# Kernel tuning notes

Measured on AMD Instinct MI355X. Metric: run time of the kernel, lower is better.

Reference implementation:

```python
import jax, jax.numpy as jnp
import numpy as np

N2 = 524288   # raw batch (2B)
F = 256       # raw feature dim; concat of halves -> D = 2F
D = 512       # input_dim (gated feature dim)
H_GATE = 64
H_EXP = 128


def _init(key, shape, fan_in):
    return jax.random.normal(key, shape, jnp.float32) / np.sqrt(fan_in)


def setup_inputs() -> dict:
    key = jax.random.key(0)
    ks = jax.random.split(key, 13)
    x = jax.random.normal(ks[0], (N2, F), jnp.float32)
    # gate: Linear(D,64) -> ReLU -> Linear(64,2)
    gw1 = _init(ks[1], (D, H_GATE), D)
    gb1 = jnp.zeros((H_GATE,), jnp.float32)
    gw2 = _init(ks[2], (H_GATE, 2), H_GATE)
    gb2 = jnp.zeros((2,), jnp.float32)
    # expert_a: Linear(D,128) -> ReLU -> Linear(128,2)
    aw1 = _init(ks[3], (D, H_EXP), D)
    ab1 = jnp.zeros((H_EXP,), jnp.float32)
    aw2 = _init(ks[4], (H_EXP, 2), H_EXP)
    ab2 = jnp.zeros((2,), jnp.float32)
    # expert_b: same shapes
    bw1 = _init(ks[5], (D, H_EXP), D)
    bb1 = jnp.zeros((H_EXP,), jnp.float32)
    bw2 = _init(ks[6], (H_EXP, 2), H_EXP)
    bb2 = jnp.zeros((2,), jnp.float32)
    return dict(x=x, gw1=gw1, gb1=gb1, gw2=gw2, gb2=gb2,
                aw1=aw1, ab1=ab1, aw2=aw2, ab2=ab2,
                bw1=bw1, bb1=bb1, bw2=bw2, bb2=bb2)


def reference(x, gw1, gb1, gw2, gb2, aw1, ab1, aw2, ab2, bw1, bb1, bw2, bb2):
    # backbone = identity; concat first and second batch halves along features
    n = x.shape[0]
    xf = jnp.concatenate([x[: n // 2], x[n // 2 :]], axis=1)  # [B, D]
    # hard gate: argmax over 2 logits
    gate_logits = jax.nn.relu(xf @ gw1 + gb1) @ gw2 + gb2  # [B, 2]
    gate_idx = jnp.argmax(gate_logits, axis=1)  # [B]
    # run both tiny experts densely, then mask (same math as masked dispatch)
    out_a = jax.nn.relu(xf @ aw1 + ab1) @ aw2 + ab2  # [B, 2]
    out_b = jax.nn.relu(xf @ bw1 + bb1) @ bw2 + bb2  # [B, 2]
    m_a = (gate_idx == 0)[:, None]
    # rows routed to expert_a fill cols 0:2, rows routed to expert_b fill cols 2:4
    return jnp.concatenate(
        [jnp.where(m_a, out_a, 0.0), jnp.where(m_a, 0.0, out_b)], axis=1
    )  # [B, 4]
```

## Files before the change

### kernel.cpp

```cpp
#include <hip/hip_runtime.h>
#include <hip/hip_bf16.h>

#define HALF_ROWS 262144
#define TAU 0.04f
#define BT_OFF 1024
#define LIST_OFF (BT_OFF + 320 * 512 * 2)
#define NC 16

typedef __attribute__((ext_vector_type(8))) short s16x8;
typedef __attribute__((ext_vector_type(4))) float f32x4;

__device__ __forceinline__ unsigned short f2bf(float f) {
  union { float f; unsigned u; } v; v.f = f;
  unsigned r = v.u + 0x7fffu + ((v.u >> 16) & 1u);
  return (unsigned short)(r >> 16);
}

#define GLOAD_LDS16(g, p) \
  __builtin_amdgcn_global_load_lds((const __attribute__((address_space(1))) void*)(g), \
                                   (__attribute__((address_space(3))) void*)(p), 16, 0, 0)

__device__ __forceinline__ s16x8 cvt8(const f32x4& a, const f32x4& b) {
  union { int i[4]; s16x8 v; } u;
  asm("v_cvt_pk_bf16_f32 %0, %1, %2" : "=v"(u.i[0]) : "v"(a[0]), "v"(a[1]));
  asm("v_cvt_pk_bf16_f32 %0, %1, %2" : "=v"(u.i[1]) : "v"(a[2]), "v"(a[3]));
  asm("v_cvt_pk_bf16_f32 %0, %1, %2" : "=v"(u.i[2]) : "v"(b[0]), "v"(b[1]));
  asm("v_cvt_pk_bf16_f32 %0, %1, %2" : "=v"(u.i[3]) : "v"(b[2]), "v"(b[3]));
  return u.v;
}

__global__ void moe_prep(const float* __restrict__ gw1, const float* __restrict__ aw1,
                         const float* __restrict__ bw1, unsigned short* __restrict__ Bf,
                         unsigned* __restrict__ cnt) {
  if (blockIdx.x == 0 && threadIdx.x == 0) *cnt = 0u;
  int idx = blockIdx.x * 512 + threadIdx.x;
  int j = idx & 7, l = (idx >> 3) & 63, ks = (idx >> 9) & 15, cb = idx >> 13;
  int col = cb * 16 + (l & 15);
  int k = ks * 32 + ((l >> 4) << 3) + j;
  float v;
  if (col < 64)       v = gw1[k * 64 + col];
  else if (col < 192) v = aw1[k * 128 + (col - 64)];
  else                v = bw1[k * 128 + (col - 192)];
  Bf[idx] = f2bf(v);
}

__global__ __launch_bounds__(768, 3) void moe_main(
    const float* __restrict__ x, const unsigned short* __restrict__ Bf,
    const float* __restrict__ gb1, const float* __restrict__ gw2, const float* __restrict__ gb2,
    const float* __restrict__ ab1, const float* __restrict__ aw2, const float* __restrict__ ab2,
    const float* __restrict__ bb1, const float* __restrict__ bw2, const float* __restrict__ bb2,
    float* __restrict__ out, unsigned* __restrict__ cnt, unsigned* __restrict__ list, int cap) {
  __shared__ char Asl[2][8192];
  __shared__ char Bsl[3][20480];

  const int tid = threadIdx.x;
  const int w = tid >> 6, l = tid & 63;
  const int lo = l & 15, hi = l >> 4;
  const long br = (long)blockIdx.x * 128;

  if (w < 4) {
    const float* apg0 = x + (br + w * 32 + lo) * 256 + hi * 8;
    const unsigned short* bsrc = Bf + l * 8;
    const int cb0 = w * 5;

    f32x4 sA[4], sB[4];
#define ISSUE_A(KC, S)                                                             \
    {                                                                              \
      const float* pb = ((KC) < 8) ? apg0 : (apg0 + (long)HALF_ROWS * 256);        \
      const float* p0 = pb + ((KC) & 7) * 32;                                      \
      const float* p1 = p0 + 16 * 256;                                             \
      asm volatile("global_load_dwordx4 %0, %1, off" : "=&v"(S[0]) : "v"(p0));     \
      asm volatile("global_load_dwordx4 %0, %1, off" : "=&v"(S[1]) : "v"(p0 + 4)); \
      asm volatile("global_load_dwordx4 %0, %1, off" : "=&v"(S[2]) : "v"(p1));     \
      asm volatile("global_load_dwordx4 %0, %1, off" : "=&v"(S[3]) : "v"(p1 + 4)); \
    }
    auto issueB = [&](int kc) {
      char* dst = Bsl[((unsigned)kc) % 3u] + cb0 * 1024;
#pragma unroll
      for (int s = 0; s < 5; ++s)
        GLOAD_LDS16(bsrc + (((size_t)((cb0 + s) * 16 + kc)) << 9), dst + s * 1024);
    };
#define COMMIT_A(KC, S)                                                            \
    {                                                                              \
      char* dst = Asl[(KC) & 1];                                                   \
      s16x8 v0 = cvt8(S[0], S[1]);                                                 \
      s16x8 v1 = cvt8(S[2], S[3]);                                                 \
      *(s16x8*)(dst + (w * 2) * 1024 + l * 16) = v0;                               \
      *(s16x8*)(dst + (w * 2 + 1) * 1024 + l * 16) = v1;                           \
    }
#define PWAIT(N) asm volatile("s_waitcnt vmcnt(" #N ")" ::: "memory"); \
                 __builtin_amdgcn_sched_barrier(0)
#define PBAR()   asm volatile("s_waitcnt lgkmcnt(0)" ::: "memory");    \
                 __builtin_amdgcn_s_barrier()

    ISSUE_A(0, sA) issueB(0);
    ISSUE_A(1, sB) issueB(1);
    PWAIT(9);
    COMMIT_A(0, sA)
    PBAR();

#pragma unroll 1
    for (int kc = 0; kc < 14; kc += 2) {
      ISSUE_A(kc + 2, sA) issueB(kc + 2);
      PWAIT(9);
      COMMIT_A(kc + 1, sB)
      PBAR();
      if (kc + 3 < NC) {
        ISSUE_A(kc + 3, sB) issueB(kc + 3);
        PWAIT(9);
      } else {
        PWAIT(0);
      }
      COMMIT_A(kc + 2, sA)
      PBAR();
    }
    PWAIT(0);
    COMMIT_A(15, sB)
    PBAR();
  } else {
    const int cw = w - 4;
    f32x4 acc[20];
#pragma unroll
    for (int ct = 0; ct < 20; ++ct) acc[ct] = (f32x4){0.f, 0.f, 0.f, 0.f};

#pragma unroll 1
    for (int kc = 0; kc < NC; ++kc) {
      __builtin_amdgcn_s_barrier();
      asm volatile("" ::: "memory");
      const char* ab = Asl[kc & 1];
      const char* bb = Bsl[((unsigned)kc) % 3u];
      s16x8 af = *(const s16x8*)(ab + cw * 1024 + l * 16);
#pragma unroll
      for (int ct = 0; ct < 20; ++ct) {
        s16x8 bf = *(const s16x8*)(bb + ct * 1024 + l * 16);
        acc[ct] = __builtin_amdgcn_mfma_f32_16x16x32_bf16(af, bf, acc[ct], 0, 0, 0);
      }
    }

    float pg0[4] = {0,0,0,0}, pg1[4] = {0,0,0,0};
    float pa0[4] = {0,0,0,0}, pa1[4] = {0,0,0,0};
    float pq0[4] = {0,0,0,0}, pq1[4] = {0,0,0,0};
#pragma unroll
    for (int ct = 0; ct < 20; ++ct) {
      int col = ct * 16 + lo;
      float b1, w0, w1;
      if (ct < 4)       { b1 = gb1[col];        w0 = gw2[col * 2];        w1 = gw2[col * 2 + 1]; }
      else if (ct < 12) { int c = col - 64;  b1 = ab1[c]; w0 = aw2[c * 2]; w1 = aw2[c * 2 + 1]; }
      else              { int c = col - 192; b1 = bb1[c]; w0 = bw2[c * 2]; w1 = bw2[c * 2 + 1]; }
#pragma unroll
      for (int j = 0; j < 4; ++j) {
        float h = fmaxf(acc[ct][j] + b1, 0.f);
        float t0 = h * w0, t1 = h * w1;
        if (ct < 4)       { pg0[j] += t0; pg1[j] += t1; }
        else if (ct < 12) { pa0[j] += t0; pa1[j] += t1; }
        else              { pq0[j] += t0; pq1[j] += t1; }
      }
    }
#pragma unroll
    for (int m = 1; m < 16; m <<= 1)
#pragma unroll
      for (int j = 0; j < 4; ++j) {
        pg0[j] += __shfl_xor(pg0[j], m); pg1[j] += __shfl_xor(pg1[j], m);
        pa0[j] += __shfl_xor(pa0[j], m); pa1[j] += __shfl_xor(pa1[j], m);
        pq0[j] += __shfl_xor(pq0[j], m); pq1[j] += __shfl_xor(pq1[j], m);
      }
    if (lo == 0) {
#pragma unroll
      for (int j = 0; j < 4; ++j) {
        long grow = br + cw * 16 + hi * 4 + j;
        float gl0 = pg0[j] + gb2[0], gl1 = pg1[j] + gb2[1];
        float fa0 = pa0[j] + ab2[0], fa1 = pa1[j] + ab2[1];
        float fb0 = pq0[j] + bb2[0], fb1 = pq1[j] + bb2[1];
        bool m0 = gl0 >= gl1;
        f32x4 o;
        o[0] = m0 ? fa0 : 0.f; o[1] = m0 ? fa1 : 0.f;
        o[2] = m0 ? 0.f : fb0; o[3] = m0 ? 0.f : fb1;
        *(f32x4*)(out + grow * 4) = o;
        float diff = gl0 - gl1;
        if (fabsf(diff) < TAU && cap > 0) {
          unsigned u = atomicAdd(cnt, 1u);
          if (u < (unsigned)cap) {
            unsigned* e = list + (size_t)u * 8;
            e[0] = (unsigned)grow;
            float* ef = (float*)(e + 4);
            ef[0] = fa0; ef[1] = fa1; ef[2] = fb0; ef[3] = fb1;
          }
        }
      }
    }
  }
}

__global__ void moe_fixup(const float* __restrict__ x,
                          const float* __restrict__ gw1, const float* __restrict__ gb1,
                          const float* __restrict__ gw2, const float* __restrict__ gb2,
                          float* __restrict__ out, const unsigned* __restrict__ cnt,
                          const unsigned* __restrict__ list, int cap) {
  unsigned n = *cnt;
  if (n > (unsigned)cap) n = (unsigned)cap;
  const int l = threadIdx.x & 63;
  const int wid = blockIdx.x * (blockDim.x >> 6) + (threadIdx.x >> 6);
  const int nw = gridDim.x * (blockDim.x >> 6);
  for (unsigned e = wid; e < n; e += nw) {
    const unsigned* ent = list + (size_t)e * 8;
    unsigned row = ent[0];
    const float* ef = (const float*)(ent + 4);
    const float* xr0 = x + (long)row * 256;
    const float* xr1 = x + ((long)row + HALF_ROWS) * 256;
    double a[8] = {0, 0, 0, 0, 0, 0, 0, 0};
#pragma unroll 2
    for (int d = 0; d < 256; d += 8)
#pragma unroll
      for (int q = 0; q < 8; ++q)
        a[q] += (double)xr0[d + q] * (double)gw1[(d + q) * 64 + l];
#pragma unroll 2
    for (int d = 0; d < 256; d += 8)
#pragma unroll
      for (int q = 0; q < 8; ++q)
        a[q] += (double)xr1[d + q] * (double)gw1[(d + 256 + q) * 64 + l];
    double h = ((a[0] + a[1]) + (a[2] + a[3])) + ((a[4] + a[5]) + (a[6] + a[7]))
             + (double)gb1[l];
    h = h > 0.0 ? h : 0.0;
    double t0 = h * (double)gw2[l * 2];
    double t1 = h * (double)gw2[l * 2 + 1];
#pragma unroll
    for (int m = 1; m < 64; m <<= 1) {
      t0 += __shfl_xor(t0, m);
      t1 += __shfl_xor(t1, m);
    }
    if (l == 0) {
      bool m0 = (t0 + (double)gb2[0]) >= (t1 + (double)gb2[1]);
      f32x4 o;
      o[0] = m0 ? ef[0] : 0.f; o[1] = m0 ? ef[1] : 0.f;
      o[2] = m0 ? 0.f : ef[2]; o[3] = m0 ? 0.f : ef[3];
      *(f32x4*)(out + (size_t)row * 4) = o;
    }
  }
}

extern "C" void kernel_launch(void* const* d_in, const int* in_sizes, int n_in,
                              void* d_out, int out_size, void* d_ws, size_t ws_size,
                              hipStream_t stream) {
  const float* x   = (const float*)d_in[0];
  const float* gw1 = (const float*)d_in[1];
  const float* gb1 = (const float*)d_in[2];
  const float* gw2 = (const float*)d_in[3];
  const float* gb2 = (const float*)d_in[4];
  const float* aw1 = (const float*)d_in[5];
  const float* ab1 = (const float*)d_in[6];
  const float* aw2 = (const float*)d_in[7];
  const float* ab2 = (const float*)d_in[8];
  const float* bw1 = (const float*)d_in[9];
  const float* bb1 = (const float*)d_in[10];
  const float* bw2 = (const float*)d_in[11];
  const float* bb2 = (const float*)d_in[12];
  float* out = (float*)d_out;

  unsigned char* ws = (unsigned char*)d_ws;
  unsigned* cnt = (unsigned*)ws;
  unsigned short* Bf = (unsigned short*)(ws + BT_OFF);
  unsigned* list = (unsigned*)(ws + LIST_OFF);
  long cap_l = ((long)ws_size - (long)LIST_OFF) / 32;
  int cap = cap_l < 0 ? 0 : (cap_l > 262144 ? 262144 : (int)cap_l);

  moe_prep<<<320, 512, 0, stream>>>(gw1, aw1, bw1, Bf, cnt);
  moe_main<<<2048, 768, 0, stream>>>(x, Bf, gb1, gw2, gb2, ab1, aw2, ab2,
                                     bb1, bw2, bb2, out, cnt, list, cap);
  moe_fixup<<<2048, 256, 0, stream>>>(x, gw1, gb1, gw2, gb2, out, cnt, list, cap);
}
```

Baseline: 285.2 us.

## Switch to 32x32x16 MFMA with split column halves and a combine kernel

The compute waves now use 32x32x16 bf16 MFMA tiles instead of 16x16x32. Each wave owns 32 rows by 160 hidden columns, and the A/B LDS layouts and the weight pre-pack are reordered to match. This cuts LDS fragment reads per MFMA and uses larger, more efficient matrix instructions. Because each row's hidden columns are now split across two waves, per-row partial second-layer sums go to a workspace buffer. A new combine kernel adds the partials, applies the gate, writes the output and builds the near-tie fixup list, at the cost of an extra launch and roughly 16 MB of extra global traffic.

```diff
diff --git a/kernel.cpp b/kernel.cpp
--- a/kernel.cpp
+++ b/kernel.cpp
@@ -4,11 +4,14 @@
 #define HALF_ROWS 262144
 #define TAU 0.04f
 #define BT_OFF 1024
-#define LIST_OFF (BT_OFF + 320 * 512 * 2)
+#define LIST_OFF 328704
+#define PART_OFF 16777216
+#define CAP 262144
 #define NC 16
 
 typedef __attribute__((ext_vector_type(8))) short s16x8;
 typedef __attribute__((ext_vector_type(4))) float f32x4;
+typedef __attribute__((ext_vector_type(16))) float f32x16;
 
 __device__ __forceinline__ unsigned short f2bf(float f) {
   union { float f; unsigned u; } v; v.f = f;
@@ -34,9 +37,9 @@
                          unsigned* __restrict__ cnt) {
   if (blockIdx.x == 0 && threadIdx.x == 0) *cnt = 0u;
   int idx = blockIdx.x * 512 + threadIdx.x;
-  int j = idx & 7, l = (idx >> 3) & 63, ks = (idx >> 9) & 15, cb = idx >> 13;
-  int col = cb * 16 + (l & 15);
-  int k = ks * 32 + ((l >> 4) << 3) + j;
+  int j = idx & 7, l = (idx >> 3) & 63, kst = (idx >> 9) & 31, cb = idx >> 14;
+  int col = cb * 32 + (l & 31);
+  int k = kst * 16 + ((l >> 5) << 3) + j;
   float v;
   if (col < 64)       v = gw1[k * 64 + col];
   else if (col < 192) v = aw1[k * 128 + (col - 64)];
@@ -46,47 +49,48 @@
 
 __global__ __launch_bounds__(768, 3) void moe_main(
     const float* __restrict__ x, const unsigned short* __restrict__ Bf,
-    const float* __restrict__ gb1, const float* __restrict__ gw2, const float* __restrict__ gb2,
-    const float* __restrict__ ab1, const float* __restrict__ aw2, const float* __restrict__ ab2,
-    const float* __restrict__ bb1, const float* __restrict__ bw2, const float* __restrict__ bb2,
-    float* __restrict__ out, unsigned* __restrict__ cnt, unsigned* __restrict__ list, int cap) {
+    const float* __restrict__ gb1, const float* __restrict__ gw2,
+    const float* __restrict__ ab1, const float* __restrict__ aw2,
+    const float* __restrict__ bb1, const float* __restrict__ bw2,
+    float* __restrict__ part) {
   __shared__ char Asl[2][8192];
   __shared__ char Bsl[3][20480];
 
   const int tid = threadIdx.x;
   const int w = tid >> 6, l = tid & 63;
-  const int lo = l & 15, hi = l >> 4;
   const long br = (long)blockIdx.x * 128;
 
   if (w < 4) {
-    const float* apg0 = x + (br + w * 32 + lo) * 256 + hi * 8;
+    const float* apg = x + (br + w * 32 + (l & 31)) * 256 + ((l >> 5) << 3);
     const unsigned short* bsrc = Bf + l * 8;
-    const int cb0 = w * 5;
+    const int s0 = w * 5;
 
     f32x4 sA[4], sB[4];
 #define ISSUE_A(KC, S)                                                             \
     {                                                                              \
-      const float* pb = ((KC) < 8) ? apg0 : (apg0 + (long)HALF_ROWS * 256);        \
+      const float* pb = ((KC) < 8) ? apg : (apg + (long)HALF_ROWS * 256);          \
       const float* p0 = pb + ((KC) & 7) * 32;                                      \
-      const float* p1 = p0 + 16 * 256;                                             \
       asm volatile("global_load_dwordx4 %0, %1, off" : "=&v"(S[0]) : "v"(p0));     \
       asm volatile("global_load_dwordx4 %0, %1, off" : "=&v"(S[1]) : "v"(p0 + 4)); \
-      asm volatile("global_load_dwordx4 %0, %1, off" : "=&v"(S[2]) : "v"(p1));     \
-      asm volatile("global_load_dwordx4 %0, %1, off" : "=&v"(S[3]) : "v"(p1 + 4)); \
+      asm volatile("global_load_dwordx4 %0, %1, off" : "=&v"(S[2]) : "v"(p0 + 16));\
+      asm volatile("global_load_dwordx4 %0, %1, off" : "=&v"(S[3]) : "v"(p0 + 20));\
     }
     auto issueB = [&](int kc) {
-      char* dst = Bsl[((unsigned)kc) % 3u] + cb0 * 1024;
-#pragma unroll
-      for (int s = 0; s < 5; ++s)
-        GLOAD_LDS16(bsrc + (((size_t)((cb0 + s) * 16 + kc)) << 9), dst + s * 1024);
+      char* dst = Bsl[((unsigned)kc) % 3u] + s0 * 1024;
+#pragma unroll
+      for (int i = 0; i < 5; ++i) {
+        int s = s0 + i;
+        GLOAD_LDS16(bsrc + (((size_t)((s >> 1) * 32 + kc * 2 + (s & 1))) << 9),
+                    dst + i * 1024);
+      }
     };
 #define COMMIT_A(KC, S)                                                            \
     {                                                                              \
       char* dst = Asl[(KC) & 1];                                                   \
       s16x8 v0 = cvt8(S[0], S[1]);                                                 \
       s16x8 v1 = cvt8(S[2], S[3]);                                                 \
-      *(s16x8*)(dst + (w * 2) * 1024 + l * 16) = v0;                               \
-      *(s16x8*)(dst + (w * 2 + 1) * 1024 + l * 16) = v1;                           \
+      *(s16x8*)(dst + ((w * 2) * 64 + l) * 16) = v0;                               \
+      *(s16x8*)(dst + ((w * 2 + 1) * 64 + l) * 16) = v1;                           \
     }
 #define PWAIT(N) asm volatile("s_waitcnt vmcnt(" #N ")" ::: "memory"); \
                  __builtin_amdgcn_sched_barrier(0)
@@ -118,10 +122,15 @@
     COMMIT_A(15, sB)
     PBAR();
   } else {
-    const int cw = w - 4;
-    f32x4 acc[20];
-#pragma unroll
-    for (int ct = 0; ct < 20; ++ct) acc[ct] = (f32x4){0.f, 0.f, 0.f, 0.f};
+    const int c = w - 4;
+    const int ch = c >> 2, g = c & 3;
+    const int lo32 = l & 31, hi2 = l >> 5;
+
+    f32x16 acc[5];
+#pragma unroll
+    for (int t = 0; t < 5; ++t)
+#pragma unroll
+      for (int q = 0; q < 16; ++q) acc[t][q] = 0.f;
 
 #pragma unroll 1
     for (int kc = 0; kc < NC; ++kc) {
@@ -129,64 +138,83 @@
       asm volatile("" ::: "memory");
       const char* ab = Asl[kc & 1];
       const char* bb = Bsl[((unsigned)kc) % 3u];
-      s16x8 af = *(const s16x8*)(ab + cw * 1024 + l * 16);
-#pragma unroll
-      for (int ct = 0; ct < 20; ++ct) {
-        s16x8 bf = *(const s16x8*)(bb + ct * 1024 + l * 16);
-        acc[ct] = __builtin_amdgcn_mfma_f32_16x16x32_bf16(af, bf, acc[ct], 0, 0, 0);
-      }
-    }
-
-    float pg0[4] = {0,0,0,0}, pg1[4] = {0,0,0,0};
-    float pa0[4] = {0,0,0,0}, pa1[4] = {0,0,0,0};
-    float pq0[4] = {0,0,0,0}, pq1[4] = {0,0,0,0};
-#pragma unroll
-    for (int ct = 0; ct < 20; ++ct) {
-      int col = ct * 16 + lo;
+      s16x8 a0 = *(const s16x8*)(ab + ((g * 2) * 64 + l) * 16);
+      s16x8 a1 = *(const s16x8*)(ab + ((g * 2 + 1) * 64 + l) * 16);
+#pragma unroll
+      for (int t = 0; t < 5; ++t) {
+        int seg = (ch * 5 + t) * 2;
+        s16x8 b0 = *(const s16x8*)(bb + (seg * 64 + l) * 16);
+        s16x8 b1f = *(const s16x8*)(bb + ((seg + 1) * 64 + l) * 16);
+        acc[t] = __builtin_amdgcn_mfma_f32_32x32x16_bf16(a0, b0, acc[t], 0, 0, 0);
+        acc[t] = __builtin_amdgcn_mfma_f32_32x32x16_bf16(a1, b1f, acc[t], 0, 0, 0);
+      }
+    }
+
+    float pg0[16], pg1[16], pa0[16], pa1[16], pq0[16], pq1[16];
+#pragma unroll
+    for (int q = 0; q < 16; ++q) {
+      pg0[q] = pg1[q] = pa0[q] = pa1[q] = pq0[q] = pq1[q] = 0.f;
+    }
+#pragma unroll
+    for (int t = 0; t < 5; ++t) {
+      int col = ch * 160 + t * 32 + lo32;
+      int c0 = ch * 160 + t * 32;
       float b1, w0, w1;
-      if (ct < 4)       { b1 = gb1[col];        w0 = gw2[col * 2];        w1 = gw2[col * 2 + 1]; }
-      else if (ct < 12) { int c = col - 64;  b1 = ab1[c]; w0 = aw2[c * 2]; w1 = aw2[c * 2 + 1]; }
-      else              { int c = col - 192; b1 = bb1[c]; w0 = bw2[c * 2]; w1 = bw2[c * 2 + 1]; }
-#pragma unroll
-      for (int j = 0; j < 4; ++j) {
-        float h = fmaxf(acc[ct][j] + b1, 0.f);
+      if (c0 < 64)       { b1 = gb1[col];        w0 = gw2[col * 2];        w1 = gw2[col * 2 + 1]; }
+      else if (c0 < 192) { int cc = col - 64;  b1 = ab1[cc]; w0 = aw2[cc * 2]; w1 = aw2[cc * 2 + 1]; }
+      else               { int cc = col - 192; b1 = bb1[cc]; w0 = bw2[cc * 2]; w1 = bw2[cc * 2 + 1]; }
+#pragma unroll
+      for (int q = 0; q < 16; ++q) {
+        float h = fmaxf(acc[t][q] + b1, 0.f);
         float t0 = h * w0, t1 = h * w1;
-        if (ct < 4)       { pg0[j] += t0; pg1[j] += t1; }
-        else if (ct < 12) { pa0[j] += t0; pa1[j] += t1; }
-        else              { pq0[j] += t0; pq1[j] += t1; }
-      }
-    }
-#pragma unroll
-    for (int m = 1; m < 16; m <<= 1)
-#pragma unroll
-      for (int j = 0; j < 4; ++j) {
-        pg0[j] += __shfl_xor(pg0[j], m); pg1[j] += __shfl_xor(pg1[j], m);
-        pa0[j] += __shfl_xor(pa0[j], m); pa1[j] += __shfl_xor(pa1[j], m);
-        pq0[j] += __shfl_xor(pq0[j], m); pq1[j] += __shfl_xor(pq1[j], m);
-      }
-    if (lo == 0) {
-#pragma unroll
-      for (int j = 0; j < 4; ++j) {
-        long grow = br + cw * 16 + hi * 4 + j;
-        float gl0 = pg0[j] + gb2[0], gl1 = pg1[j] + gb2[1];
-        float fa0 = pa0[j] + ab2[0], fa1 = pa1[j] + ab2[1];
-        float fb0 = pq0[j] + bb2[0], fb1 = pq1[j] + bb2[1];
-        bool m0 = gl0 >= gl1;
-        f32x4 o;
-        o[0] = m0 ? fa0 : 0.f; o[1] = m0 ? fa1 : 0.f;
-        o[2] = m0 ? 0.f : fb0; o[3] = m0 ? 0.f : fb1;
-        *(f32x4*)(out + grow * 4) = o;
-        float diff = gl0 - gl1;
-        if (fabsf(diff) < TAU && cap > 0) {
-          unsigned u = atomicAdd(cnt, 1u);
-          if (u < (unsigned)cap) {
-            unsigned* e = list + (size_t)u * 8;
-            e[0] = (unsigned)grow;
-            float* ef = (float*)(e + 4);
-            ef[0] = fa0; ef[1] = fa1; ef[2] = fb0; ef[3] = fb1;
-          }
-        }
-      }
+        if (c0 < 64)       { pg0[q] += t0; pg1[q] += t1; }
+        else if (c0 < 192) { pa0[q] += t0; pa1[q] += t1; }
+        else               { pq0[q] += t0; pq1[q] += t1; }
+      }
+    }
+#pragma unroll
+    for (int m = 1; m < 32; m <<= 1)
+#pragma unroll
+      for (int q = 0; q < 16; ++q) {
+        pg0[q] += __shfl_xor(pg0[q], m); pg1[q] += __shfl_xor(pg1[q], m);
+        pa0[q] += __shfl_xor(pa0[q], m); pa1[q] += __shfl_xor(pa1[q], m);
+        pq0[q] += __shfl_xor(pq0[q], m); pq1[q] += __shfl_xor(pq1[q], m);
+      }
+    if (lo32 == 0) {
+#pragma unroll
+      for (int q = 0; q < 16; ++q) {
+        long row = br + g * 32 + (q & 3) + 8 * (q >> 2) + 4 * hi2;
+        float* pp = part + ((long)ch * 262144 + row) * 8;
+        pp[0] = pg0[q]; pp[1] = pg1[q]; pp[2] = pa0[q];
+        pp[3] = pa1[q]; pp[4] = pq0[q]; pp[5] = pq1[q];
+      }
+    }
+  }
+}
+
+__global__ void moe_combine(const float* __restrict__ part,
+                            const float* __restrict__ gb2, const float* __restrict__ ab2,
+                            const float* __restrict__ bb2, float* __restrict__ out,
+                            unsigned* __restrict__ cnt, unsigned* __restrict__ list, int cap) {
+  long r = (long)blockIdx.x * 256 + threadIdx.x;
+  const float* p0 = part + r * 8;
+  const float* p1 = part + (262144L + r) * 8;
+  float gl0 = p0[0] + gb2[0], gl1 = p0[1] + gb2[1];
+  float fa0 = p0[2] + p1[2] + ab2[0], fa1 = p0[3] + p1[3] + ab2[1];
+  float fb0 = p1[4] + bb2[0], fb1 = p1[5] + bb2[1];
+  bool m0 = gl0 >= gl1;
+  f32x4 o;
+  o[0] = m0 ? fa0 : 0.f; o[1] = m0 ? fa1 : 0.f;
+  o[2] = m0 ? 0.f : fb0; o[3] = m0 ? 0.f : fb1;
+  *(f32x4*)(out + r * 4) = o;
+  float diff = gl0 - gl1;
+  if (fabsf(diff) < TAU && cap > 0) {
+    unsigned u = atomicAdd(cnt, 1u);
+    if (u < (unsigned)cap) {
+      unsigned* e = list + (size_t)u * 8;
+      e[0] = (unsigned)r;
+      float* ef = (float*)(e + 4);
+      ef[0] = fa0; ef[1] = fa1; ef[2] = fb0; ef[3] = fb1;
     }
   }
 }
@@ -260,11 +288,11 @@
   unsigned* cnt = (unsigned*)ws;
   unsigned short* Bf = (unsigned short*)(ws + BT_OFF);
   unsigned* list = (unsigned*)(ws + LIST_OFF);
-  long cap_l = ((long)ws_size - (long)LIST_OFF) / 32;
-  int cap = cap_l < 0 ? 0 : (cap_l > 262144 ? 262144 : (int)cap_l);
+  float* part = (float*)(ws + PART_OFF);
+  int cap = (ws_size >= PART_OFF + 2L * 262144 * 32) ? CAP : 0;
 
   moe_prep<<<320, 512, 0, stream>>>(gw1, aw1, bw1, Bf, cnt);
-  moe_main<<<2048, 768, 0, stream>>>(x, Bf, gb1, gw2, gb2, ab1, aw2, ab2,
-                                     bb1, bw2, bb2, out, cnt, list, cap);
+  moe_main<<<2048, 768, 0, stream>>>(x, Bf, gb1, gw2, ab1, aw2, bb1, bw2, part);
+  moe_combine<<<1024, 256, 0, stream>>>(part, gb2, ab2, bb2, out, cnt, list, cap);
   moe_fixup<<<2048, 256, 0, stream>>>(x, gw1, gb1, gw2, gb2, out, cnt, list, cap);
 }
```

Result: slower. 489.6 us (+71.7%).
